# Performance work log

Measured on AMD Instinct MI355X. Metric: run time of the kernel, lower is better.

Reference implementation:

```python
import jax, jax.numpy as jnp
import numpy as np

B, L, V, D = 4096, 128, 50257, 64
NEG_INF = -1e9
COS_EPS = 1e-8  # torch cosine_similarity default eps


def setup_inputs() -> dict:
    key = jax.random.key(0)
    k1, k2, k3, k4, k5, k6 = jax.random.split(key, 6)
    return {
        "ids_a": jax.random.randint(k1, (B, L), 0, V, dtype=jnp.int64) if jax.config.jax_enable_x64 else jax.random.randint(k1, (B, L), 0, V, dtype=jnp.int32),
        "mask_a": jax.random.randint(k2, (B, L), 0, 2, dtype=jnp.int32),
        "ids_b": jax.random.randint(k3, (B, L), 0, V, dtype=jnp.int32),
        "mask_b": jax.random.randint(k4, (B, L), 0, 2, dtype=jnp.int32),
        "mu_table": jax.random.normal(k5, (V, D), dtype=jnp.float32),
        "feat_table": jax.random.normal(k6, (V, D), dtype=jnp.float32),
    }


def _side(ids, mask, mu_table, feat_table):
    # Embedding gathers: [B, L, D]
    mu = mu_table[ids]
    feat = feat_table[ids]
    m = mask.astype(mu.dtype)  # [B, L]
    # render_mean_pool: masked mean of mu -> query [B, D]
    denom = jnp.maximum(m.sum(axis=1, keepdims=True), 1.0)
    q = jnp.einsum('bld,bl->bd', mu, m) / denom
    # render_softmax_attention: single-query masked softmax over mu keys
    scores = jnp.einsum('bld,bd->bl', mu, q)
    scores = jnp.where(mask.astype(bool), scores, NEG_INF)
    attn = jax.nn.softmax(scores, axis=-1)  # [B, L]
    return jnp.einsum('bl,bld->bd', attn, feat)  # weighted sum of feat


def reference(ids_a, mask_a, ids_b, mask_b, mu_table, feat_table):
    mean_a = _side(ids_a, mask_a, mu_table, feat_table)
    mean_b = _side(ids_b, mask_b, mu_table, feat_table)
    # torch cosine_similarity: x.y / (max(||x||, eps) * max(||y||, eps))
    na = jnp.maximum(jnp.linalg.norm(mean_a, axis=-1), COS_EPS)
    nb = jnp.maximum(jnp.linalg.norm(mean_b, axis=-1), COS_EPS)
    cos = jnp.sum(mean_a * mean_b, axis=-1) / (na * nb)
    return cos * 5.0
```

## Files before the change

### kernel.cpp

```cpp
#include <hip/hip_runtime.h>
#include <hip/hip_fp16.h>
#include <math.h>

#define BB 4096
#define LL 128
#define DD 64
#define VV 50257
#define TAB_ELEMS (VV * DD)

typedef _Float16 h2_t __attribute__((ext_vector_type(2)));

__device__ __forceinline__ float dot2acc(unsigned a, unsigned b, float c) {
#if __has_builtin(__builtin_amdgcn_fdot2)
    return __builtin_amdgcn_fdot2(__builtin_bit_cast(h2_t, a),
                                  __builtin_bit_cast(h2_t, b), c, false);
#else
    const float2 fa = __half22float2(*(const __half2*)&a);
    const float2 fb = __half22float2(*(const __half2*)&b);
    return fmaf(fa.x, fb.x, fmaf(fa.y, fb.y, c));
#endif
}

__device__ __forceinline__ float2 cvt2(unsigned raw) {
    return __half22float2(*(const __half2*)&raw);
}

__device__ __forceinline__ unsigned pack_h2(float a, float b) {
    union { __half2 h; unsigned u; } p;
    p.h = __floats2half2_rn(a, b);
    return p.u;
}

__global__ __launch_bounds__(256) void convert_fused_kernel(
    const float* __restrict__ mu, const float* __restrict__ feat,
    __half* __restrict__ out)
{
    const int total = VV * 16;
    for (int i = blockIdx.x * blockDim.x + threadIdx.x; i < total;
         i += gridDim.x * blockDim.x) {
        const int row = i >> 4;
        const int c   = i & 15;
        const float* src = (c < 8) ? (mu   + row * DD + c * 8)
                                   : (feat + row * DD + (c - 8) * 8);
        const float4 s0 = ((const float4*)src)[0];
        const float4 s1 = ((const float4*)src)[1];
        uint4 o;
        o.x = pack_h2(s0.x, s0.y); o.y = pack_h2(s0.z, s0.w);
        o.z = pack_h2(s1.x, s1.y); o.w = pack_h2(s1.z, s1.w);
        ((uint4*)out)[i] = o;
    }
}

__global__ __launch_bounds__(256, 4) void softmax_attn_cos_kernel(
    const int* __restrict__ ids_a, const int* __restrict__ mask_a,
    const int* __restrict__ ids_b, const int* __restrict__ mask_b,
    const __half* __restrict__ fused_table, float* __restrict__ out)
{
    __shared__ int      s_cid[2][LL];
    __shared__ int      s_cnt[2][2];
    __shared__ unsigned s_qh[2][32];
    __shared__ float4   s_qp[2][2][16];
    __shared__ float    s_sc[2][LL];
    __shared__ float4   s_op[2][2][16];
    __shared__ float    s_mean[2][DD];
    __shared__ float    s_sum[2];

    const int tid  = threadIdx.x;
    const int lane = tid & 63;
    const int wave = tid >> 6;
    const int side = wave >> 1;
    const int wsub = wave & 1;
    const int r8   = lane >> 3;
    const int c8   = lane & 7;
    const int b    = blockIdx.x;

    {
        const int l = wsub * 64 + lane;
        const int* idp = side ? ids_b  : ids_a;
        const int* mp  = side ? mask_b : mask_a;
        const int id = idp[b * LL + l];
        const int m  = mp[b * LL + l];
        const unsigned long long bal = __ballot(m != 0);
        if (lane == 0) s_cnt[side][wsub] = __popcll(bal);
        const int rank = __popcll(bal & ((1ull << lane) - 1ull));
        __syncthreads();
        const int offset = wsub ? s_cnt[side][0] : 0;
        if (m) s_cid[side][offset + rank] = id;
        if (s_cnt[side][0] + s_cnt[side][1] == 0)
            s_cid[side][l] = id;
    }
    __syncthreads();

    const int   nm  = s_cnt[side][0] + s_cnt[side][1];
    const int   nme = (nm == 0) ? 128 : nm;
    const int   G   = (nme + 7) >> 3;

    uint4 v[8];
    uint4 f[8];
    {
        #pragma unroll
        for (int it = 0; it < 8; ++it) {
            v[it] = make_uint4(0u, 0u, 0u, 0u);
            f[it] = make_uint4(0u, 0u, 0u, 0u);
            const int g = 2 * it + wsub;
            if (g < G) {
                const int p  = g * 8 + r8;
                const int id = (p < nme) ? s_cid[side][p] : 0;
                const char* base = (const char*)fused_table
                                 + ((unsigned)id << 8) + ((unsigned)c8 << 4);
                v[it] = *(const uint4*)(base);
                f[it] = *(const uint4*)(base + 128);
            }
        }
        float4 qa = make_float4(0.f, 0.f, 0.f, 0.f);
        float4 qb = make_float4(0.f, 0.f, 0.f, 0.f);
        #pragma unroll
        for (int it = 0; it < 8; ++it) {
            const int g = 2 * it + wsub;
            const int p = g * 8 + r8;
            if (g < G && p < nm) {
                const float2 f0 = cvt2(v[it].x), f1 = cvt2(v[it].y);
                const float2 f2 = cvt2(v[it].z), f3 = cvt2(v[it].w);
                qa.x += f0.x; qa.y += f0.y; qa.z += f1.x; qa.w += f1.y;
                qb.x += f2.x; qb.y += f2.y; qb.z += f3.x; qb.w += f3.y;
            }
        }
        #pragma unroll
        for (int off = 8; off <= 32; off <<= 1) {
            qa.x += __shfl_xor(qa.x, off, 64); qa.y += __shfl_xor(qa.y, off, 64);
            qa.z += __shfl_xor(qa.z, off, 64); qa.w += __shfl_xor(qa.w, off, 64);
            qb.x += __shfl_xor(qb.x, off, 64); qb.y += __shfl_xor(qb.y, off, 64);
            qb.z += __shfl_xor(qb.z, off, 64); qb.w += __shfl_xor(qb.w, off, 64);
        }
        if (lane < 8) {
            s_qp[side][wsub][2 * c8]     = qa;
            s_qp[side][wsub][2 * c8 + 1] = qb;
        }
    }
    __syncthreads();

    if (tid < 128) {
        const int si = tid >> 6;
        const int dd = tid & 63;
        if (dd < 16) {
            const float dn = fmaxf((float)(s_cnt[si][0] + s_cnt[si][1]), 1.0f);
            const float rd = 1.0f / dn;
            const float4 q0 = s_qp[si][0][dd], q1 = s_qp[si][1][dd];
            s_qh[si][2 * dd]     = pack_h2((q0.x + q1.x) * rd, (q0.y + q1.y) * rd);
            s_qh[si][2 * dd + 1] = pack_h2((q0.z + q1.z) * rd, (q0.w + q1.w) * rd);
        }
    }
    __syncthreads();

    {
        const uint4 qq = ((const uint4*)&s_qh[side][0])[c8];
        #pragma unroll
        for (int it = 0; it < 8; ++it) {
            const int g = 2 * it + wsub;
            if (g < G) {
                const int p = g * 8 + r8;
                float sp = dot2acc(v[it].x, qq.x, 0.f);
                sp = dot2acc(v[it].y, qq.y, sp);
                sp = dot2acc(v[it].z, qq.z, sp);
                sp = dot2acc(v[it].w, qq.w, sp);
                #pragma unroll
                for (int off = 1; off <= 4; off <<= 1)
                    sp += __shfl_xor(sp, off, 64);
                if (c8 == 0 && p < nme) s_sc[side][p] = sp;
            }
        }
    }
    __syncthreads();

    if (wsub == 0) {
        const float s1 = (lane      < nme) ? s_sc[side][lane]      : -1e9f;
        const float s2 = (lane + 64 < nme) ? s_sc[side][lane + 64] : -1e9f;
        float mx = fmaxf(s1, s2);
        #pragma unroll
        for (int off = 32; off; off >>= 1) mx = fmaxf(mx, __shfl_xor(mx, off, 64));
        const float e1 = expf(s1 - mx), e2 = expf(s2 - mx);
        s_sc[side][lane] = e1; s_sc[side][lane + 64] = e2;
        float sm = e1 + e2;
        #pragma unroll
        for (int off = 32; off; off >>= 1) sm += __shfl_xor(sm, off, 64);
        if (lane == 0) s_sum[side] = sm;
    }
    __syncthreads();

    {
        float4 oa = make_float4(0.f, 0.f, 0.f, 0.f);
        float4 ob = make_float4(0.f, 0.f, 0.f, 0.f);
        #pragma unroll
        for (int it = 0; it < 8; ++it) {
            const int g = 2 * it + wsub;
            if (g < G) {
                const int p = g * 8 + r8;
                const float w = (p < nme) ? s_sc[side][p] : 0.f;
                const float2 f0 = cvt2(f[it].x), f1 = cvt2(f[it].y);
                const float2 f2 = cvt2(f[it].z), f3 = cvt2(f[it].w);
                oa.x = fmaf(f0.x, w, oa.x); oa.y = fmaf(f0.y, w, oa.y);
                oa.z = fmaf(f1.x, w, oa.z); oa.w = fmaf(f1.y, w, oa.w);
                ob.x = fmaf(f2.x, w, ob.x); ob.y = fmaf(f2.y, w, ob.y);
                ob.z = fmaf(f3.x, w, ob.z); ob.w = fmaf(f3.y, w, ob.w);
            }
        }
        #pragma unroll
        for (int off = 8; off <= 32; off <<= 1) {
            oa.x += __shfl_xor(oa.x, off, 64); oa.y += __shfl_xor(oa.y, off, 64);
            oa.z += __shfl_xor(oa.z, off, 64); oa.w += __shfl_xor(oa.w, off, 64);
            ob.x += __shfl_xor(ob.x, off, 64); ob.y += __shfl_xor(ob.y, off, 64);
            ob.z += __shfl_xor(ob.z, off, 64); ob.w += __shfl_xor(ob.w, off, 64);
        }
        if (lane < 8) {
            s_op[side][wsub][2 * c8]     = oa;
            s_op[side][wsub][2 * c8 + 1] = ob;
        }
    }
    __syncthreads();

    if (tid < 32) {
        const int si = tid >> 4, cc = tid & 15;
        const float inv = 1.0f / s_sum[si];
        const float4 o0 = s_op[si][0][cc], o1 = s_op[si][1][cc];
        float4 o;
        o.x = (o0.x + o1.x) * inv; o.y = (o0.y + o1.y) * inv;
        o.z = (o0.z + o1.z) * inv; o.w = (o0.w + o1.w) * inv;
        ((float4*)&s_mean[si][0])[cc] = o;
    }
    __syncthreads();

    if (tid < 64) {
        const float a = s_mean[0][tid], c = s_mean[1][tid];
        float dt = a * c, na = a * a, nb = c * c;
        #pragma unroll
        for (int off = 32; off; off >>= 1) {
            dt += __shfl_xor(dt, off, 64);
            na += __shfl_xor(na, off, 64);
            nb += __shfl_xor(nb, off, 64);
        }
        if (tid == 0) {
            const float denom = fmaxf(sqrtf(na), 1e-8f) * fmaxf(sqrtf(nb), 1e-8f);
            out[b] = 5.0f * dt / denom;
        }
    }
}

extern "C" void kernel_launch(void* const* d_in, const int* in_sizes, int n_in,
                              void* d_out, int out_size, void* d_ws, size_t ws_size,
                              hipStream_t stream) {
    const int*   ids_a  = (const int*)d_in[0];
    const int*   mask_a = (const int*)d_in[1];
    const int*   ids_b  = (const int*)d_in[2];
    const int*   mask_b = (const int*)d_in[3];
    const float* mu     = (const float*)d_in[4];
    const float* feat   = (const float*)d_in[5];
    float* out = (float*)d_out;

    __half* ws_fused = (__half*)d_ws;

    convert_fused_kernel<<<2048, 256, 0, stream>>>(mu, feat, ws_fused);
    softmax_attn_cos_kernel<<<BB, 256, 0, stream>>>(
        ids_a, mask_a, ids_b, mask_b, ws_fused, out);
}
```

Before: 112.5 us.

## Drop fp16 table pre-conversion; gather fp32 rows directly and convert in registers

Removes the separate kernel that converted both full embedding tables to a fused fp16 workspace every call. The main kernel now gathers fp32 mu and feat rows straight from the input tables, sums the query from the fp32 values, and packs them to fp16 in registers for the later stages. This removes a full pass over roughly 25 MB of tables plus a launch, at the cost of gathering twice as many bytes per token (512 B instead of 256 B per row) and some extra register pressure.

```diff
diff --git a/kernel.cpp b/kernel.cpp
--- a/kernel.cpp
+++ b/kernel.cpp
@@ -6,7 +6,6 @@
 #define LL 128
 #define DD 64
 #define VV 50257
-#define TAB_ELEMS (VV * DD)
 
 typedef _Float16 h2_t __attribute__((ext_vector_type(2)));
 
@@ -31,30 +30,11 @@
     return p.u;
 }
 
-__global__ __launch_bounds__(256) void convert_fused_kernel(
-    const float* __restrict__ mu, const float* __restrict__ feat,
-    __half* __restrict__ out)
-{
-    const int total = VV * 16;
-    for (int i = blockIdx.x * blockDim.x + threadIdx.x; i < total;
-         i += gridDim.x * blockDim.x) {
-        const int row = i >> 4;
-        const int c   = i & 15;
-        const float* src = (c < 8) ? (mu   + row * DD + c * 8)
-                                   : (feat + row * DD + (c - 8) * 8);
-        const float4 s0 = ((const float4*)src)[0];
-        const float4 s1 = ((const float4*)src)[1];
-        uint4 o;
-        o.x = pack_h2(s0.x, s0.y); o.y = pack_h2(s0.z, s0.w);
-        o.z = pack_h2(s1.x, s1.y); o.w = pack_h2(s1.z, s1.w);
-        ((uint4*)out)[i] = o;
-    }
-}
-
 __global__ __launch_bounds__(256, 4) void softmax_attn_cos_kernel(
     const int* __restrict__ ids_a, const int* __restrict__ mask_a,
     const int* __restrict__ ids_b, const int* __restrict__ mask_b,
-    const __half* __restrict__ fused_table, float* __restrict__ out)
+    const float* __restrict__ mu_table, const float* __restrict__ feat_table,
+    float* __restrict__ out)
 {
     __shared__ int      s_cid[2][LL];
     __shared__ int      s_cnt[2][2];
@@ -98,6 +78,8 @@
     uint4 v[8];
     uint4 f[8];
     {
+        float4 qa = make_float4(0.f, 0.f, 0.f, 0.f);
+        float4 qb = make_float4(0.f, 0.f, 0.f, 0.f);
         #pragma unroll
         for (int it = 0; it < 8; ++it) {
             v[it] = make_uint4(0u, 0u, 0u, 0u);
@@ -106,23 +88,19 @@
             if (g < G) {
                 const int p  = g * 8 + r8;
                 const int id = (p < nme) ? s_cid[side][p] : 0;
-                const char* base = (const char*)fused_table
-                                 + ((unsigned)id << 8) + ((unsigned)c8 << 4);
-                v[it] = *(const uint4*)(base);
-                f[it] = *(const uint4*)(base + 128);
-            }
-        }
-        float4 qa = make_float4(0.f, 0.f, 0.f, 0.f);
-        float4 qb = make_float4(0.f, 0.f, 0.f, 0.f);
-        #pragma unroll
-        for (int it = 0; it < 8; ++it) {
-            const int g = 2 * it + wsub;
-            const int p = g * 8 + r8;
-            if (g < G && p < nm) {
-                const float2 f0 = cvt2(v[it].x), f1 = cvt2(v[it].y);
-                const float2 f2 = cvt2(v[it].z), f3 = cvt2(v[it].w);
-                qa.x += f0.x; qa.y += f0.y; qa.z += f1.x; qa.w += f1.y;
-                qb.x += f2.x; qb.y += f2.y; qb.z += f3.x; qb.w += f3.y;
+                const unsigned byo = ((unsigned)id << 8) + ((unsigned)c8 << 5);
+                const float4 m0 = *(const float4*)((const char*)mu_table   + byo);
+                const float4 m1 = *(const float4*)((const char*)mu_table   + byo + 16);
+                const float4 g0 = *(const float4*)((const char*)feat_table + byo);
+                const float4 g1 = *(const float4*)((const char*)feat_table + byo + 16);
+                if (p < nm) {
+                    qa.x += m0.x; qa.y += m0.y; qa.z += m0.z; qa.w += m0.w;
+                    qb.x += m1.x; qb.y += m1.y; qb.z += m1.z; qb.w += m1.w;
+                }
+                v[it].x = pack_h2(m0.x, m0.y); v[it].y = pack_h2(m0.z, m0.w);
+                v[it].z = pack_h2(m1.x, m1.y); v[it].w = pack_h2(m1.z, m1.w);
+                f[it].x = pack_h2(g0.x, g0.y); f[it].y = pack_h2(g0.z, g0.w);
+                f[it].z = pack_h2(g1.x, g1.y); f[it].w = pack_h2(g1.z, g1.w);
             }
         }
         #pragma unroll
@@ -255,10 +233,8 @@
     const float* mu     = (const float*)d_in[4];
     const float* feat   = (const float*)d_in[5];
     float* out = (float*)d_out;
-
-    __half* ws_fused = (__half*)d_ws;
-
-    convert_fused_kernel<<<2048, 256, 0, stream>>>(mu, feat, ws_fused);
+    (void)d_ws; (void)ws_size;
+
     softmax_attn_cos_kernel<<<BB, 256, 0, stream>>>(
-        ids_a, mask_a, ids_b, mask_b, ws_fused, out);
-}
+        ids_a, mask_a, ids_b, mask_b, mu, feat, out);
+}
```

After: 118.1 us. 1.05x slower.
